# Performance work log

Hardware: AMD Instinct MI355X
Metric: run time of the kernel (lower is better)

Reference implementation:

```python
import jax, jax.numpy as jnp
import numpy as np

N_EMITTERS = 200000
N_FRAMES = 500


def setup_inputs() -> dict:
    key = jax.random.key(0)
    k1, _ = jax.random.split(key)
    # initial state must be one-hot per emitter: column 0 = 'on', column 1 = 'off'
    on = jax.random.bernoulli(k1, 0.5, (N_EMITTERS,))
    initial = jnp.stack([on, ~on], axis=-1).astype(jnp.float32)  # [N, 2] one-hot
    # transition[j] is the categorical distribution over {stay-ish, flip-ish} given row j
    transition = jnp.array([[0.5, 0.5], [0.9, 0.1]], dtype=jnp.float32)
    # transition_matrix[0] = identity (keep state), transition_matrix[1] = swap (flip state)
    transition_matrix = jnp.array([[[1.0, 0.0], [0.0, 1.0]],
                                   [[0.0, 1.0], [1.0, 0.0]]], dtype=jnp.float32)
    return {"initial": initial, "transition": transition,
            "transition_matrix": transition_matrix, "n_frames": N_FRAMES}


def reference(initial, transition, transition_matrix, n_frames):
    # Faithful translation of the per-frame Python loop as a single lax.scan.
    # Original: A = Cat(transition).sample([N]) -> A[n, j] ~ Cat(transition[j, :]) in {0, 1}
    #           t = (state * A).sum(-1)   (selects A at the current one-hot state index)
    #           state = state @ transition_matrix[t]
    # Output: per-frame on-mask (original returned np.where(state[:, 0] == 1) indices,
    # which has data-dependent shape; we return the equivalent dense mask).
    p1 = transition[:, 1]  # prob of drawing class 1 for each of the 2 row-distributions
    keys = jax.random.split(jax.random.key(42), n_frames)

    def step(state, k):
        u = jax.random.uniform(k, (state.shape[0], 2), dtype=state.dtype)  # [N, 2]
        A = (u < p1[None, :]).astype(state.dtype)  # categorical sample per row dist, {0,1}
        t = jnp.sum(state * A, axis=-1).astype(jnp.int32)  # [N] chosen action per emitter
        m = transition_matrix[t]  # [N, 2, 2] identity-or-swap
        new_state = jnp.einsum('ni,nij->nj', state, m)  # [N, 2] one-hot update
        return new_state, new_state[:, 0]

    _, on_mask = jax.lax.scan(step, initial, keys)
    return on_mask  # [n_frames, N], 1.0 where emitter is in the 'on' state
```

## Files before the change

### kernel.cpp

```cpp
#include <hip/hip_runtime.h>
#include <stdint.h>


#define ROTL32(x, d) __builtin_amdgcn_alignbit((x), (x), 32 - (d))

__device__ __forceinline__ void tf2x32(uint32_t k0, uint32_t k1,
                                       uint32_t x0, uint32_t x1,
                                       uint32_t& o0, uint32_t& o1) {
  const uint32_t k2 = k0 ^ k1 ^ 0x1BD11BDAu;
  x0 += k0; x1 += k1;
#define TF_R(d) { x0 += x1; x1 = ROTL32(x1, d) ^ x0; }
  TF_R(13) TF_R(15) TF_R(26) TF_R(6)
  x0 += k1; x1 += k2 + 1u;
  TF_R(17) TF_R(29) TF_R(16) TF_R(24)
  x0 += k2; x1 += k0 + 2u;
  TF_R(13) TF_R(15) TF_R(26) TF_R(6)
  x0 += k0; x1 += k1 + 3u;
  TF_R(17) TF_R(29) TF_R(16) TF_R(24)
  x0 += k1; x1 += k2 + 4u;
  TF_R(13) TF_R(15) TF_R(26) TF_R(6)
  x0 += k2; x1 += k0 + 5u;
#undef TF_R
  o0 = x0; o1 = x1;
}

__global__ void subkeys_kernel(uint2* __restrict__ ks, int nf, int cap) {
  const int f = blockIdx.x * blockDim.x + threadIdx.x;
  if (f < nf) {
    uint32_t a, b;
    tf2x32(0u, 42u, 0u, (uint32_t)f, a, b);
    ks[f] = make_uint2(a, b);
  } else if (f < cap) {
    ks[f] = make_uint2(0u, 0u);
  }
}

__device__ __forceinline__ uint32_t cipher(uint32_t k0, uint32_t k1,
                                           uint32_t x1in) {
  const uint32_t k2 = k0 ^ k1 ^ 0x1BD11BDAu;
  const uint32_t c1 = k2 + 1u, c2 = k0 + 2u, c3 = k1 + 3u,
                 c4 = k2 + 4u, c5 = k0 + 5u;

  uint32_t x0 = k0 + x1in;
  uint32_t x1 = ROTL32(x1in, 13) ^ x0;
  x0 += x1; x1 = ROTL32(x1, 15) ^ x0;
  x0 += x1; x1 = ROTL32(x1, 26) ^ x0;
  x0 += x1; x1 = ROTL32(x1,  6) ^ x0;
  x1 += c1; x0 = x0 + k1 + x1;
  x1 = ROTL32(x1, 17) ^ x0;
  x0 += x1; x1 = ROTL32(x1, 29) ^ x0;
  x0 += x1; x1 = ROTL32(x1, 16) ^ x0;
  x0 += x1; x1 = ROTL32(x1, 24) ^ x0;
  x1 += c2; x0 = x0 + k2 + x1;
  x1 = ROTL32(x1, 13) ^ x0;
  x0 += x1; x1 = ROTL32(x1, 15) ^ x0;
  x0 += x1; x1 = ROTL32(x1, 26) ^ x0;
  x0 += x1; x1 = ROTL32(x1,  6) ^ x0;
  x1 += c3; x0 = x0 + k0 + x1;
  x1 = ROTL32(x1, 17) ^ x0;
  x0 += x1; x1 = ROTL32(x1, 29) ^ x0;
  x0 += x1; x1 = ROTL32(x1, 16) ^ x0;
  x0 += x1; x1 = ROTL32(x1, 24) ^ x0;
  x1 += c4; x0 = x0 + k1 + x1;
  x1 = ROTL32(x1, 13) ^ x0;
  x0 += x1; x1 = ROTL32(x1, 15) ^ x0;
  x0 += x1; x1 = ROTL32(x1, 26) ^ x0;
  x0 += x1; x1 = ROTL32(x1,  6) ^ x0;
  return (x0 + k2) ^ (x1 + c5);
}

__device__ __forceinline__ void run_fast(
    const uint2* __restrict__ ks, float* __restrict__ out, int n, int N,
    int nf, bool s, uint32_t tsh0, uint32_t tsh1) {
  const uint32_t base = 2u * (uint32_t)n;
  uint32_t thr = s ? tsh1 : tsh0;
  float* col = out;

  const int ng = nf / 8;
  for (int g = 0; g < ng; ++g) {
    const int f0 = g * 8;
    uint2 k[8];
#pragma unroll
    for (int i = 0; i < 8; ++i) k[i] = ks[f0 + i];

    uint32_t vals[8];
#pragma unroll
    for (int i = 0; i < 8; ++i) {
      const uint32_t x1in = base + (s ? 1u : 0u) + k[i].y;
      const uint32_t r = cipher(k[i].x, k[i].y, x1in);
      s = s != (r < thr);
      thr = s ? tsh1 : tsh0;
      vals[i] = s ? 0u : 0x3f800000u;
    }
#pragma unroll
    for (int i = 0; i < 8; ++i) {
      __builtin_nontemporal_store(vals[i], (uint32_t*)(col + (size_t)i * N) + n);
    }
    col += (size_t)8 * N;
  }
  for (int f = ng * 8; f < nf; ++f) {
    const uint2 kk = ks[f];
    const uint32_t x1in = base + (s ? 1u : 0u) + kk.y;
    const uint32_t r = cipher(kk.x, kk.y, x1in);
    s = s != (r < thr);
    thr = s ? tsh1 : tsh0;
    __builtin_nontemporal_store(s ? 0u : 0x3f800000u, (uint32_t*)col + n);
    col += N;
  }
}

__device__ __forceinline__ void run_general(
    const uint2* __restrict__ ks, float* __restrict__ out, int n, int N,
    int nf, uint32_t s, uint32_t tsh0, uint32_t tsh1,
    uint32_t sw0, uint32_t sw1) {
  const uint32_t base = 2u * (uint32_t)n;
  uint32_t thr = s ? tsh1 : tsh0;
  float* col = out;
  for (int f = 0; f < nf; ++f) {
    const uint2 kk = ks[f];
    const uint32_t r = cipher(kk.x, kk.y, base + s + kk.y);
    s ^= (r < thr) ? sw1 : sw0;
    thr = s ? tsh1 : tsh0;
    __builtin_nontemporal_store(s ? 0u : 0x3f800000u, (uint32_t*)col + n);
    col += N;
  }
}

__device__ __forceinline__ void markov_body(
    const float* __restrict__ initial, const float* __restrict__ transition,
    const float* __restrict__ tmat, const uint2* __restrict__ ks,
    float* __restrict__ out, int N, int nf) {
  const int n = blockIdx.x * blockDim.x + threadIdx.x;
  if (n >= N) return;

  const uint64_t t0w = ((uint64_t)(uint32_t)ceilf(transition[1] * 8388608.0f)) << 9;
  const uint64_t t1w = ((uint64_t)(uint32_t)ceilf(transition[3] * 8388608.0f)) << 9;
  const uint32_t tsh0 = (t0w > 0xFFFFFFFFull) ? 0xFFFFFFFFu : (uint32_t)t0w;
  const uint32_t tsh1 = (t1w > 0xFFFFFFFFull) ? 0xFFFFFFFFu : (uint32_t)t1w;
  const uint32_t sw0 = (tmat[1] != 0.0f) ? 1u : 0u;
  const uint32_t sw1 = (tmat[5] != 0.0f) ? 1u : 0u;

  const bool s0 = (initial[2 * n] == 0.0f);

  if (sw0 == 0u && sw1 == 1u) {
    run_fast(ks, out, n, N, nf, s0, tsh0, tsh1);
  } else {
    run_general(ks, out, n, N, nf, s0 ? 1u : 0u, tsh0, tsh1, sw0, sw1);
  }
}

__global__ __launch_bounds__(256) void markov_kernel(
    const float* __restrict__ initial, const float* __restrict__ transition,
    const float* __restrict__ tmat, const uint2* __restrict__ ks,
    float* __restrict__ out, int N, int nf) {
  markov_body(initial, transition, tmat, ks, out, N, nf);
}

__global__ __launch_bounds__(256) void markov_kernel_lds(
    const float* __restrict__ initial, const float* __restrict__ transition,
    const float* __restrict__ tmat, float* __restrict__ out,
    int N, int nf, int cap) {
  extern __shared__ uint2 kf[];
  for (int f = threadIdx.x; f < cap; f += blockDim.x) {
    uint2 k = make_uint2(0u, 0u);
    if (f < nf) {
      uint32_t a, b;
      tf2x32(0u, 42u, 0u, (uint32_t)f, a, b);
      k = make_uint2(a, b);
    }
    kf[f] = k;
  }
  __syncthreads();
  markov_body(initial, transition, tmat, kf, out, N, nf);
}

extern "C" void kernel_launch(void* const* d_in, const int* in_sizes, int n_in,
                              void* d_out, int out_size, void* d_ws, size_t ws_size,
                              hipStream_t stream) {
  const float* initial    = (const float*)d_in[0];
  const float* transition = (const float*)d_in[1];
  const float* tmat       = (const float*)d_in[2];
  float* out = (float*)d_out;

  const int N  = in_sizes[0] / 2;
  const int nf = (N > 0) ? (out_size / N) : 0;
  if (N <= 0 || nf <= 0) return;

  const int block = 256;
  const int grid = (N + block - 1) / block;

  const int cap = ((nf + 7) / 8 + 1) * 8;
  const size_t need = (size_t)cap * sizeof(uint2);
  if (ws_size >= need) {
    uint2* ks = (uint2*)d_ws;
    subkeys_kernel<<<(cap + 255) / 256, 256, 0, stream>>>(ks, nf, cap);
    markov_kernel<<<grid, block, 0, stream>>>(initial, transition, tmat, ks,
                                              out, N, nf);
  } else {
    markov_kernel_lds<<<grid, block, need, stream>>>(initial, transition,
                                                     tmat, out, N, nf, cap);
  }
}
```

Measured before the change: 265.6 us.

## Process three or four emitters per thread with shared per-frame key constants

Launches a fixed-size grid where each thread advances three (or four) independent emitter chains, hoisting the per-frame Threefry key schedule out of the per-emitter cipher. This increases instruction-level parallelism and amortizes key setup across chains. In exchange, stores become strided across lanes, occupancy drops to roughly one block per CU, and the specialized swap fast path is replaced by the general update.

```diff
diff --git a/kernel.cpp b/kernel.cpp
--- a/kernel.cpp
+++ b/kernel.cpp
@@ -36,11 +36,10 @@
 }
 
 __device__ __forceinline__ uint32_t cipher(uint32_t k0, uint32_t k1,
+                                           uint32_t k2, uint32_t c1,
+                                           uint32_t c2, uint32_t c3,
+                                           uint32_t c4, uint32_t c5,
                                            uint32_t x1in) {
-  const uint32_t k2 = k0 ^ k1 ^ 0x1BD11BDAu;
-  const uint32_t c1 = k2 + 1u, c2 = k0 + 2u, c3 = k1 + 3u,
-                 c4 = k2 + 4u, c5 = k0 + 5u;
-
   uint32_t x0 = k0 + x1in;
   uint32_t x1 = ROTL32(x1in, 13) ^ x0;
   x0 += x1; x1 = ROTL32(x1, 15) ^ x0;
@@ -69,94 +68,122 @@
   return (x0 + k2) ^ (x1 + c5);
 }
 
-__device__ __forceinline__ void run_fast(
-    const uint2* __restrict__ ks, float* __restrict__ out, int n, int N,
-    int nf, bool s, uint32_t tsh0, uint32_t tsh1) {
-  const uint32_t base = 2u * (uint32_t)n;
-  uint32_t thr = s ? tsh1 : tsh0;
-  float* col = out;
-
-  const int ng = nf / 8;
+template <int NC>
+__device__ __forceinline__ void run_nc(
+    const uint2* __restrict__ ks, float* __restrict__ out,
+    const uint32_t* __restrict__ base, const int* __restrict__ noff,
+    uint32_t* __restrict__ s, int N, int nf,
+    uint32_t tsh0, uint32_t tsh1, uint32_t sw0, uint32_t sw1) {
+  uint32_t thr[NC];
+#pragma unroll
+  for (int j = 0; j < NC; ++j) thr[j] = s[j] ? tsh1 : tsh0;
+
+  const int ng = nf / 4;
   for (int g = 0; g < ng; ++g) {
-    const int f0 = g * 8;
-    uint2 k[8];
-#pragma unroll
-    for (int i = 0; i < 8; ++i) k[i] = ks[f0 + i];
-
-    uint32_t vals[8];
-#pragma unroll
-    for (int i = 0; i < 8; ++i) {
-      const uint32_t x1in = base + (s ? 1u : 0u) + k[i].y;
-      const uint32_t r = cipher(k[i].x, k[i].y, x1in);
-      s = s != (r < thr);
-      thr = s ? tsh1 : tsh0;
-      vals[i] = s ? 0u : 0x3f800000u;
-    }
-#pragma unroll
-    for (int i = 0; i < 8; ++i) {
-      __builtin_nontemporal_store(vals[i], (uint32_t*)(col + (size_t)i * N) + n);
-    }
-    col += (size_t)8 * N;
-  }
-  for (int f = ng * 8; f < nf; ++f) {
+    const int f0 = 4 * g;
+    uint2 k[4];
+#pragma unroll
+    for (int i = 0; i < 4; ++i) k[i] = ks[f0 + i];
+
+    uint32_t vals[4][NC];
+#pragma unroll
+    for (int i = 0; i < 4; ++i) {
+      const uint32_t k0 = k[i].x, k1 = k[i].y;
+      const uint32_t k2 = k0 ^ k1 ^ 0x1BD11BDAu;
+      const uint32_t c1 = k2 + 1u, c2 = k0 + 2u, c3 = k1 + 3u,
+                     c4 = k2 + 4u, c5 = k0 + 5u;
+#pragma unroll
+      for (int j = 0; j < NC; ++j) {
+        const uint32_t r = cipher(k0, k1, k2, c1, c2, c3, c4, c5,
+                                  base[j] + s[j] + k1);
+        s[j] ^= (r < thr[j]) ? sw1 : sw0;
+        thr[j] = s[j] ? tsh1 : tsh0;
+        vals[i][j] = s[j] ? 0u : 0x3f800000u;
+      }
+    }
+#pragma unroll
+    for (int i = 0; i < 4; ++i) {
+      uint32_t* row = (uint32_t*)out + (size_t)(f0 + i) * N;
+#pragma unroll
+      for (int j = 0; j < NC; ++j)
+        __builtin_nontemporal_store(vals[i][j], row + noff[j]);
+    }
+  }
+  for (int f = ng * 4; f < nf; ++f) {
     const uint2 kk = ks[f];
-    const uint32_t x1in = base + (s ? 1u : 0u) + kk.y;
-    const uint32_t r = cipher(kk.x, kk.y, x1in);
-    s = s != (r < thr);
-    thr = s ? tsh1 : tsh0;
-    __builtin_nontemporal_store(s ? 0u : 0x3f800000u, (uint32_t*)col + n);
-    col += N;
-  }
-}
-
-__device__ __forceinline__ void run_general(
-    const uint2* __restrict__ ks, float* __restrict__ out, int n, int N,
-    int nf, uint32_t s, uint32_t tsh0, uint32_t tsh1,
-    uint32_t sw0, uint32_t sw1) {
-  const uint32_t base = 2u * (uint32_t)n;
-  uint32_t thr = s ? tsh1 : tsh0;
-  float* col = out;
-  for (int f = 0; f < nf; ++f) {
-    const uint2 kk = ks[f];
-    const uint32_t r = cipher(kk.x, kk.y, base + s + kk.y);
-    s ^= (r < thr) ? sw1 : sw0;
-    thr = s ? tsh1 : tsh0;
-    __builtin_nontemporal_store(s ? 0u : 0x3f800000u, (uint32_t*)col + n);
-    col += N;
-  }
-}
-
-__device__ __forceinline__ void markov_body(
+    const uint32_t k0 = kk.x, k1 = kk.y;
+    const uint32_t k2 = k0 ^ k1 ^ 0x1BD11BDAu;
+    const uint32_t c1 = k2 + 1u, c2 = k0 + 2u, c3 = k1 + 3u,
+                   c4 = k2 + 4u, c5 = k0 + 5u;
+    uint32_t* row = (uint32_t*)out + (size_t)f * N;
+#pragma unroll
+    for (int j = 0; j < NC; ++j) {
+      const uint32_t r = cipher(k0, k1, k2, c1, c2, c3, c4, c5,
+                                base[j] + s[j] + k1);
+      s[j] ^= (r < thr[j]) ? sw1 : sw0;
+      thr[j] = s[j] ? tsh1 : tsh0;
+      __builtin_nontemporal_store(s[j] ? 0u : 0x3f800000u, row + noff[j]);
+    }
+  }
+}
+
+__device__ __forceinline__ void get_params(
+    const float* transition, const float* tmat,
+    uint32_t& tsh0, uint32_t& tsh1, uint32_t& sw0, uint32_t& sw1) {
+  const uint64_t t0w = ((uint64_t)(uint32_t)ceilf(transition[1] * 8388608.0f)) << 9;
+  const uint64_t t1w = ((uint64_t)(uint32_t)ceilf(transition[3] * 8388608.0f)) << 9;
+  tsh0 = (t0w > 0xFFFFFFFFull) ? 0xFFFFFFFFu : (uint32_t)t0w;
+  tsh1 = (t1w > 0xFFFFFFFFull) ? 0xFFFFFFFFu : (uint32_t)t1w;
+  sw0 = (tmat[1] != 0.0f) ? 1u : 0u;
+  sw1 = (tmat[5] != 0.0f) ? 1u : 0u;
+}
+
+__global__ __launch_bounds__(256) void markov3_kernel(
+    const float* __restrict__ initial, const float* __restrict__ transition,
+    const float* __restrict__ tmat, const uint2* __restrict__ ks,
+    float* __restrict__ out, int N, int nf, int T, int extra) {
+  const int t = blockIdx.x * blockDim.x + threadIdx.x;
+
+  uint32_t tsh0, tsh1, sw0, sw1;
+  get_params(transition, tmat, tsh0, tsh1, sw0, sw1);
+
+  const int n0 = 3 * t;
+  uint32_t s[4];
+  uint32_t base[4];
+  int noff[4];
+#pragma unroll
+  for (int j = 0; j < 3; ++j) {
+    const int n = n0 + j;
+    s[j] = (initial[2 * n] != 0.0f) ? 0u : 1u;
+    base[j] = 2u * (uint32_t)n;
+    noff[j] = n;
+  }
+  if (t < extra) {
+    const int n3 = 3 * T + t;
+    s[3] = (initial[2 * n3] != 0.0f) ? 0u : 1u;
+    base[3] = 2u * (uint32_t)n3;
+    noff[3] = n3;
+    run_nc<4>(ks, out, base, noff, s, N, nf, tsh0, tsh1, sw0, sw1);
+  } else {
+    run_nc<3>(ks, out, base, noff, s, N, nf, tsh0, tsh1, sw0, sw1);
+  }
+}
+
+__global__ __launch_bounds__(256) void markov_generic_kernel(
     const float* __restrict__ initial, const float* __restrict__ transition,
     const float* __restrict__ tmat, const uint2* __restrict__ ks,
     float* __restrict__ out, int N, int nf) {
   const int n = blockIdx.x * blockDim.x + threadIdx.x;
   if (n >= N) return;
-
-  const uint64_t t0w = ((uint64_t)(uint32_t)ceilf(transition[1] * 8388608.0f)) << 9;
-  const uint64_t t1w = ((uint64_t)(uint32_t)ceilf(transition[3] * 8388608.0f)) << 9;
-  const uint32_t tsh0 = (t0w > 0xFFFFFFFFull) ? 0xFFFFFFFFu : (uint32_t)t0w;
-  const uint32_t tsh1 = (t1w > 0xFFFFFFFFull) ? 0xFFFFFFFFu : (uint32_t)t1w;
-  const uint32_t sw0 = (tmat[1] != 0.0f) ? 1u : 0u;
-  const uint32_t sw1 = (tmat[5] != 0.0f) ? 1u : 0u;
-
-  const bool s0 = (initial[2 * n] == 0.0f);
-
-  if (sw0 == 0u && sw1 == 1u) {
-    run_fast(ks, out, n, N, nf, s0, tsh0, tsh1);
-  } else {
-    run_general(ks, out, n, N, nf, s0 ? 1u : 0u, tsh0, tsh1, sw0, sw1);
-  }
-}
-
-__global__ __launch_bounds__(256) void markov_kernel(
-    const float* __restrict__ initial, const float* __restrict__ transition,
-    const float* __restrict__ tmat, const uint2* __restrict__ ks,
-    float* __restrict__ out, int N, int nf) {
-  markov_body(initial, transition, tmat, ks, out, N, nf);
-}
-
-__global__ __launch_bounds__(256) void markov_kernel_lds(
+  uint32_t tsh0, tsh1, sw0, sw1;
+  get_params(transition, tmat, tsh0, tsh1, sw0, sw1);
+  uint32_t s[1] = {(initial[2 * n] != 0.0f) ? 0u : 1u};
+  uint32_t base[1] = {2u * (uint32_t)n};
+  int noff[1] = {n};
+  run_nc<1>(ks, out, base, noff, s, N, nf, tsh0, tsh1, sw0, sw1);
+}
+
+__global__ __launch_bounds__(256) void markov_lds_kernel(
     const float* __restrict__ initial, const float* __restrict__ transition,
     const float* __restrict__ tmat, float* __restrict__ out,
     int N, int nf, int cap) {
@@ -171,7 +198,14 @@
     kf[f] = k;
   }
   __syncthreads();
-  markov_body(initial, transition, tmat, kf, out, N, nf);
+  const int n = blockIdx.x * blockDim.x + threadIdx.x;
+  if (n >= N) return;
+  uint32_t tsh0, tsh1, sw0, sw1;
+  get_params(transition, tmat, tsh0, tsh1, sw0, sw1);
+  uint32_t s[1] = {(initial[2 * n] != 0.0f) ? 0u : 1u};
+  uint32_t base[1] = {2u * (uint32_t)n};
+  int noff[1] = {n};
+  run_nc<1>(kf, out, base, noff, s, N, nf, tsh0, tsh1, sw0, sw1);
 }
 
 extern "C" void kernel_launch(void* const* d_in, const int* in_sizes, int n_in,
@@ -186,18 +220,29 @@
   const int nf = (N > 0) ? (out_size / N) : 0;
   if (N <= 0 || nf <= 0) return;
 
-  const int block = 256;
-  const int grid = (N + block - 1) / block;
-
-  const int cap = ((nf + 7) / 8 + 1) * 8;
+  const int cap = ((nf + 3) / 4 + 1) * 4;
   const size_t need = (size_t)cap * sizeof(uint2);
-  if (ws_size >= need) {
-    uint2* ks = (uint2*)d_ws;
-    subkeys_kernel<<<(cap + 255) / 256, 256, 0, stream>>>(ks, nf, cap);
-    markov_kernel<<<grid, block, 0, stream>>>(initial, transition, tmat, ks,
-                                              out, N, nf);
+
+  if (ws_size < need) {
+    const int block = 256;
+    const int grid = (N + block - 1) / block;
+    markov_lds_kernel<<<grid, block, need, stream>>>(initial, transition,
+                                                     tmat, out, N, nf, cap);
+    return;
+  }
+
+  uint2* ks = (uint2*)d_ws;
+  subkeys_kernel<<<(cap + 255) / 256, 256, 0, stream>>>(ks, nf, cap);
+
+  const int T = 65536;
+  if (N >= 3 * T && N < 4 * T) {
+    const int extra = N - 3 * T;
+    markov3_kernel<<<T / 256, 256, 0, stream>>>(initial, transition, tmat,
+                                                ks, out, N, nf, T, extra);
   } else {
-    markov_kernel_lds<<<grid, block, need, stream>>>(initial, transition,
-                                                     tmat, out, N, nf, cap);
-  }
-}
+    const int block = 256;
+    const int grid = (N + block - 1) / block;
+    markov_generic_kernel<<<grid, block, 0, stream>>>(initial, transition,
+                                                      tmat, ks, out, N, nf);
+  }
+}
```

After: 276.1 us. 4.0% more time.
